# Optimization experiments

Measured on AMD Instinct MI355X. Metric: run time of the kernel, lower is better.

Reference implementation:

```python
import jax, jax.numpy as jnp
import numpy as np

B, N, H = 1048576, 6, 32

def setup_inputs() -> dict:
    key = jax.random.key(0)
    k = jax.random.split(key, 6)
    return {
        "x": jax.random.normal(k[0], (B, N), dtype=jnp.float32),
        "A_param": jax.random.normal(k[1], (N, N), dtype=jnp.float32),
        "W1": jax.random.normal(k[2], (H, 1), dtype=jnp.float32) * (1.0),  # Linear(1,H) weight
        "b1": jax.random.normal(k[3], (H,), dtype=jnp.float32) * 0.1,
        "W2": jax.random.normal(k[4], (1, H), dtype=jnp.float32) * (1.0 / np.sqrt(H)),
        "b2": jax.random.normal(k[5], (1,), dtype=jnp.float32) * 0.1,
    }

def reference(x, A_param, W1, b1, W2, b2):
    # A = softmax over rows of learned adjacency  [N, N]
    A = jax.nn.softmax(A_param, axis=-1)
    # fc1: per-node scalar -> hidden  [B, N, H]
    h = x[..., None] * W1[:, 0] + b1
    # graph mixing: A @ h  [B, N, H]
    h = jnp.einsum('mn,bnh->bmh', A, h)
    h = jax.nn.relu(h)
    # fc2: hidden -> scalar, squeeze  [B, N]
    h = jnp.einsum('bnh,h->bn', h, W2[0]) + b2[0]
    return x + h
```

## Files before the change

kernel.cpp:

```cpp
#include <hip/hip_runtime.h>
#include <math.h>


typedef float f32x2 __attribute__((ext_vector_type(2)));
typedef float f32x4 __attribute__((ext_vector_type(4)));

#define NN 6
#define HH 32
#define NB 512
#define YMIN  (-8.0f)
#define YSPAN (16.0f)
#define INVH  ((float)NB / YSPAN)
#define OFFS  (-YMIN * INVH)
#define BINW  (YSPAN / (float)NB)
#define WF4   192

#define LDS_FENCE() asm volatile("s_waitcnt lgkmcnt(0)" ::: "memory")

__device__ __forceinline__ f32x2 mk2(float a, float b) {
    f32x2 r; r.x = a; r.y = b; return r;
}

__device__ __forceinline__ f32x2 pk_fma(f32x2 a, f32x2 b, f32x2 c) {
#if __has_builtin(__builtin_elementwise_fma)
    return __builtin_elementwise_fma(a, b, c);
#else
    f32x2 r; r.x = fmaf(a.x, b.x, c.x); r.y = fmaf(a.y, b.y, c.y); return r;
#endif
}

__device__ __forceinline__ void eval_pair(
    f32x4 v0, f32x4 v1, f32x4 v2,
    const float* __restrict__ sA,
    const f32x2* __restrict__ sTab,
    f32x4& o0, f32x4& o1, f32x4& o2)
{
    f32x2 xx[NN];
    xx[0] = mk2(v0.x, v1.z);
    xx[1] = mk2(v0.y, v1.w);
    xx[2] = mk2(v0.z, v2.x);
    xx[3] = mk2(v0.w, v2.y);
    xx[4] = mk2(v1.x, v2.z);
    xx[5] = mk2(v1.y, v2.w);

    f32x2 yy[NN];
#pragma unroll
    for (int m = 0; m < NN; ++m) {
        f32x2 a = mk2(0.f, 0.f);
#pragma unroll
        for (int n = 0; n < NN; ++n) {
            float c = sA[m * NN + n];
            a = pk_fma(mk2(c, c), xx[n], a);
        }
        yy[m] = a;
    }

    f32x2 rr[NN];
#pragma unroll
    for (int m = 0; m < NN; ++m) {
#pragma unroll
        for (int half = 0; half < 2; ++half) {
            float yv = half ? yy[m].y : yy[m].x;
            float fi = fmaf(yv, INVH, OFFS);
            fi = fminf(fmaxf(fi, 0.0f), (float)(NB - 1));
            int k = (int)fi;
            f32x2 ab = sTab[k];
            float r = fmaf(ab.y, yv, ab.x);
            if (half) rr[m].y = r; else rr[m].x = r;
        }
    }

    o0.x = v0.x + rr[0].x;
    o0.y = v0.y + rr[1].x;
    o0.z = v0.z + rr[2].x;
    o0.w = v0.w + rr[3].x;
    o1.x = v1.x + rr[4].x;
    o1.y = v1.y + rr[5].x;
    o1.z = v1.z + rr[0].y;
    o1.w = v1.w + rr[1].y;
    o2.x = v2.x + rr[2].y;
    o2.y = v2.y + rr[3].y;
    o2.z = v2.z + rr[4].y;
    o2.w = v2.w + rr[5].y;
}

__global__ __launch_bounds__(256, 4) void graph_block_fused(
    const float* __restrict__ x,
    const float* __restrict__ Ap,
    const float* __restrict__ W1p,
    const float* __restrict__ b1p,
    const float* __restrict__ W2p,
    const float* __restrict__ b2p,
    float* __restrict__ out,
    int nF4)
{
    __shared__ float sA[NN * NN];
    __shared__ __align__(16) f32x2 sTab[NB];
    __shared__ __align__(16) f32x4 slab[4][WF4];

    const int tid = threadIdx.x;
    const int wid = tid >> 6;
    const int lane = tid & 63;

    const f32x4* __restrict__ xv = (const f32x4*)x;
    f32x4* __restrict__ ov = (f32x4*)out;

    const int base = (blockIdx.x * 4 + wid) * (2 * WF4);

    f32x4 a0, a1, a2, c0, c1, c2;
    if (base + lane < nF4)       a0 = xv[base + lane];
    if (base + 64 + lane < nF4)  a1 = xv[base + 64 + lane];
    if (base + 128 + lane < nF4) a2 = xv[base + 128 + lane];
    if (base + 192 + lane < nF4) c0 = xv[base + 192 + lane];
    if (base + 256 + lane < nF4) c1 = xv[base + 256 + lane];
    if (base + 320 + lane < nF4) c2 = xv[base + 320 + lane];

    if (tid < NN) {
        float r[NN];
        float mx = -INFINITY;
#pragma unroll
        for (int n = 0; n < NN; ++n) {
            r[n] = Ap[tid * NN + n];
            mx = fmaxf(mx, r[n]);
        }
        float s = 0.f;
#pragma unroll
        for (int n = 0; n < NN; ++n) {
            r[n] = expf(r[n] - mx);
            s += r[n];
        }
        float inv = 1.f / s;
#pragma unroll
        for (int n = 0; n < NN; ++n) sA[tid * NN + n] = r[n] * inv;
    }

    {
        float bb2 = b2p[0];
#pragma unroll
        for (int i = 0; i < 2; ++i) {
            int k = tid + i * 256;
            float ea = YMIN + (float)k * BINW;
            float eb = ea + BINW;
            float fa = bb2, fb = bb2;
#pragma unroll
            for (int h = 0; h < HH; ++h) {
                float w1 = W1p[h], bv = b1p[h], w2 = W2p[h];
                fa = fmaf(fmaxf(fmaf(w1, ea, bv), 0.f), w2, fa);
                fb = fmaf(fmaxf(fmaf(w1, eb, bv), 0.f), w2, fb);
            }
            float beta = (fb - fa) * INVH;
            sTab[k] = mk2(fmaf(-beta, ea, fa), beta);
        }
    }
    __syncthreads();

    f32x4* sl = slab[wid];

    auto run_chunk = [&](f32x4 s0, f32x4 s1, f32x4 s2, int cb) {
        sl[lane]       = s0;
        sl[64 + lane]  = s1;
        sl[128 + lane] = s2;
        LDS_FENCE();
        f32x4 v0 = sl[3 * lane];
        f32x4 v1 = sl[3 * lane + 1];
        f32x4 v2 = sl[3 * lane + 2];
        f32x4 o0, o1, o2;
        eval_pair(v0, v1, v2, sA, sTab, o0, o1, o2);
        LDS_FENCE();
        sl[3 * lane]     = o0;
        sl[3 * lane + 1] = o1;
        sl[3 * lane + 2] = o2;
        LDS_FENCE();
        f32x4 u0 = sl[lane];
        f32x4 u1 = sl[64 + lane];
        f32x4 u2 = sl[128 + lane];
        if (cb + lane < nF4)       ov[cb + lane] = u0;
        if (cb + 64 + lane < nF4)  ov[cb + 64 + lane] = u1;
        if (cb + 128 + lane < nF4) ov[cb + 128 + lane] = u2;
        LDS_FENCE();
    };

    run_chunk(a0, a1, a2, base);
    run_chunk(c0, c1, c2, base + WF4);
}

extern "C" void kernel_launch(void* const* d_in, const int* in_sizes, int n_in,
                              void* d_out, int out_size, void* d_ws, size_t ws_size,
                              hipStream_t stream) {
    const float* x  = (const float*)d_in[0];
    const float* Ap = (const float*)d_in[1];
    const float* W1 = (const float*)d_in[2];
    const float* b1 = (const float*)d_in[3];
    const float* W2 = (const float*)d_in[4];
    const float* b2 = (const float*)d_in[5];
    float* out = (float*)d_out;

    int nF4 = in_sizes[0] / 4;
    int perBlock = 4 * 2 * WF4;
    int grid = (nF4 + perBlock - 1) / perBlock;
    graph_block_fused<<<grid, 256, 0, stream>>>(x, Ap, W1, b1, W2, b2, out, nF4);
}
```

Measured before the change: 17.65 us.

## Split table/softmax prep into separate kernel and drop LDS transposition

Moves the softmax of the adjacency and the piecewise-linear lookup table construction into a one-block prep kernel that writes them to workspace. The main kernel then has each thread load its three float4 values directly (strided per-thread loads) and reads A and the table from global memory or cache instead of LDS. This removes the per-block table rebuild, the barrier and the LDS staging shuffle. In exchange it adds a second kernel launch, gather lookups that go through cache instead of LDS, and less coalesced 48-byte-strided loads.

```diff
diff --git a/kernel.cpp b/kernel.cpp
--- a/kernel.cpp
+++ b/kernel.cpp
@@ -13,9 +13,6 @@
 #define INVH  ((float)NB / YSPAN)
 #define OFFS  (-YMIN * INVH)
 #define BINW  (YSPAN / (float)NB)
-#define WF4   192
-
-#define LDS_FENCE() asm volatile("s_waitcnt lgkmcnt(0)" ::: "memory")
 
 __device__ __forceinline__ f32x2 mk2(float a, float b) {
     f32x2 r; r.x = a; r.y = b; return r;
@@ -29,91 +26,13 @@
 #endif
 }
 
-__device__ __forceinline__ void eval_pair(
-    f32x4 v0, f32x4 v1, f32x4 v2,
-    const float* __restrict__ sA,
-    const f32x2* __restrict__ sTab,
-    f32x4& o0, f32x4& o1, f32x4& o2)
-{
-    f32x2 xx[NN];
-    xx[0] = mk2(v0.x, v1.z);
-    xx[1] = mk2(v0.y, v1.w);
-    xx[2] = mk2(v0.z, v2.x);
-    xx[3] = mk2(v0.w, v2.y);
-    xx[4] = mk2(v1.x, v2.z);
-    xx[5] = mk2(v1.y, v2.w);
-
-    f32x2 yy[NN];
-#pragma unroll
-    for (int m = 0; m < NN; ++m) {
-        f32x2 a = mk2(0.f, 0.f);
-#pragma unroll
-        for (int n = 0; n < NN; ++n) {
-            float c = sA[m * NN + n];
-            a = pk_fma(mk2(c, c), xx[n], a);
-        }
-        yy[m] = a;
-    }
-
-    f32x2 rr[NN];
-#pragma unroll
-    for (int m = 0; m < NN; ++m) {
-#pragma unroll
-        for (int half = 0; half < 2; ++half) {
-            float yv = half ? yy[m].y : yy[m].x;
-            float fi = fmaf(yv, INVH, OFFS);
-            fi = fminf(fmaxf(fi, 0.0f), (float)(NB - 1));
-            int k = (int)fi;
-            f32x2 ab = sTab[k];
-            float r = fmaf(ab.y, yv, ab.x);
-            if (half) rr[m].y = r; else rr[m].x = r;
-        }
-    }
-
-    o0.x = v0.x + rr[0].x;
-    o0.y = v0.y + rr[1].x;
-    o0.z = v0.z + rr[2].x;
-    o0.w = v0.w + rr[3].x;
-    o1.x = v1.x + rr[4].x;
-    o1.y = v1.y + rr[5].x;
-    o1.z = v1.z + rr[0].y;
-    o1.w = v1.w + rr[1].y;
-    o2.x = v2.x + rr[2].y;
-    o2.y = v2.y + rr[3].y;
-    o2.z = v2.z + rr[4].y;
-    o2.w = v2.w + rr[5].y;
-}
-
-__global__ __launch_bounds__(256, 4) void graph_block_fused(
-    const float* __restrict__ x,
-    const float* __restrict__ Ap,
-    const float* __restrict__ W1p,
-    const float* __restrict__ b1p,
-    const float* __restrict__ W2p,
-    const float* __restrict__ b2p,
-    float* __restrict__ out,
-    int nF4)
-{
-    __shared__ float sA[NN * NN];
-    __shared__ __align__(16) f32x2 sTab[NB];
-    __shared__ __align__(16) f32x4 slab[4][WF4];
-
+__global__ void prep_kernel(const float* __restrict__ Ap,
+                            const float* __restrict__ W1p,
+                            const float* __restrict__ b1p,
+                            const float* __restrict__ W2p,
+                            const float* __restrict__ b2p,
+                            float* __restrict__ ws) {
     const int tid = threadIdx.x;
-    const int wid = tid >> 6;
-    const int lane = tid & 63;
-
-    const f32x4* __restrict__ xv = (const f32x4*)x;
-    f32x4* __restrict__ ov = (f32x4*)out;
-
-    const int base = (blockIdx.x * 4 + wid) * (2 * WF4);
-
-    f32x4 a0, a1, a2, c0, c1, c2;
-    if (base + lane < nF4)       a0 = xv[base + lane];
-    if (base + 64 + lane < nF4)  a1 = xv[base + 64 + lane];
-    if (base + 128 + lane < nF4) a2 = xv[base + 128 + lane];
-    if (base + 192 + lane < nF4) c0 = xv[base + 192 + lane];
-    if (base + 256 + lane < nF4) c1 = xv[base + 256 + lane];
-    if (base + 320 + lane < nF4) c2 = xv[base + 320 + lane];
 
     if (tid < NN) {
         float r[NN];
@@ -131,57 +50,99 @@
         }
         float inv = 1.f / s;
 #pragma unroll
-        for (int n = 0; n < NN; ++n) sA[tid * NN + n] = r[n] * inv;
+        for (int n = 0; n < NN; ++n) ws[tid * NN + n] = r[n] * inv;
     }
 
-    {
-        float bb2 = b2p[0];
+    float bb2 = b2p[0];
+    f32x2* __restrict__ tab = (f32x2*)(ws + 64);
 #pragma unroll
-        for (int i = 0; i < 2; ++i) {
-            int k = tid + i * 256;
-            float ea = YMIN + (float)k * BINW;
-            float eb = ea + BINW;
-            float fa = bb2, fb = bb2;
+    for (int i = 0; i < 2; ++i) {
+        int k = tid + i * 256;
+        float ea = YMIN + (float)k * BINW;
+        float eb = ea + BINW;
+        float fa = bb2, fb = bb2;
 #pragma unroll
-            for (int h = 0; h < HH; ++h) {
-                float w1 = W1p[h], bv = b1p[h], w2 = W2p[h];
-                fa = fmaf(fmaxf(fmaf(w1, ea, bv), 0.f), w2, fa);
-                fb = fmaf(fmaxf(fmaf(w1, eb, bv), 0.f), w2, fb);
-            }
-            float beta = (fb - fa) * INVH;
-            sTab[k] = mk2(fmaf(-beta, ea, fa), beta);
+        for (int h = 0; h < HH; ++h) {
+            float w1 = W1p[h], bv = b1p[h], w2 = W2p[h];
+            fa = fmaf(fmaxf(fmaf(w1, ea, bv), 0.f), w2, fa);
+            fb = fmaf(fmaxf(fmaf(w1, eb, bv), 0.f), w2, fb);
+        }
+        float beta = (fb - fa) * INVH;
+        tab[k] = mk2(fmaf(-beta, ea, fa), beta);
+    }
+}
+
+__global__ __launch_bounds__(256, 4) void graph_block_main(
+    const float* __restrict__ x,
+    const float* __restrict__ ws,
+    float* __restrict__ out,
+    int nPairs)
+{
+    const int p = blockIdx.x * 256 + threadIdx.x;
+    if (p >= nPairs) return;
+
+    const f32x4* __restrict__ xv = (const f32x4*)x;
+    f32x4* __restrict__ ov = (f32x4*)out;
+
+    f32x4 v0 = xv[3 * p];
+    f32x4 v1 = xv[3 * p + 1];
+    f32x4 v2 = xv[3 * p + 2];
+
+    const float* __restrict__ A = ws;
+    const f32x2* __restrict__ tab = (const f32x2*)(ws + 64);
+
+    f32x2 xx[NN];
+    xx[0] = mk2(v0.x, v1.z);
+    xx[1] = mk2(v0.y, v1.w);
+    xx[2] = mk2(v0.z, v2.x);
+    xx[3] = mk2(v0.w, v2.y);
+    xx[4] = mk2(v1.x, v2.z);
+    xx[5] = mk2(v1.y, v2.w);
+
+    f32x2 yy[NN];
+#pragma unroll
+    for (int m = 0; m < NN; ++m) {
+        f32x2 a = mk2(0.f, 0.f);
+#pragma unroll
+        for (int n = 0; n < NN; ++n) {
+            float c = A[m * NN + n];
+            a = pk_fma(mk2(c, c), xx[n], a);
+        }
+        yy[m] = a;
+    }
+
+    f32x2 rr[NN];
+#pragma unroll
+    for (int m = 0; m < NN; ++m) {
+#pragma unroll
+        for (int half = 0; half < 2; ++half) {
+            float yv = half ? yy[m].y : yy[m].x;
+            float fi = fmaf(yv, INVH, OFFS);
+            fi = fminf(fmaxf(fi, 0.0f), (float)(NB - 1));
+            int k = (int)fi;
+            f32x2 ab = tab[k];
+            float r = fmaf(ab.y, yv, ab.x);
+            if (half) rr[m].y = r; else rr[m].x = r;
         }
     }
-    __syncthreads();
 
-    f32x4* sl = slab[wid];
+    f32x4 o0, o1, o2;
+    o0.x = v0.x + rr[0].x;
+    o0.y = v0.y + rr[1].x;
+    o0.z = v0.z + rr[2].x;
+    o0.w = v0.w + rr[3].x;
+    o1.x = v1.x + rr[4].x;
+    o1.y = v1.y + rr[5].x;
+    o1.z = v1.z + rr[0].y;
+    o1.w = v1.w + rr[1].y;
+    o2.x = v2.x + rr[2].y;
+    o2.y = v2.y + rr[3].y;
+    o2.z = v2.z + rr[4].y;
+    o2.w = v2.w + rr[5].y;
 
-    auto run_chunk = [&](f32x4 s0, f32x4 s1, f32x4 s2, int cb) {
-        sl[lane]       = s0;
-        sl[64 + lane]  = s1;
-        sl[128 + lane] = s2;
-        LDS_FENCE();
-        f32x4 v0 = sl[3 * lane];
-        f32x4 v1 = sl[3 * lane + 1];
-        f32x4 v2 = sl[3 * lane + 2];
-        f32x4 o0, o1, o2;
-        eval_pair(v0, v1, v2, sA, sTab, o0, o1, o2);
-        LDS_FENCE();
-        sl[3 * lane]     = o0;
-        sl[3 * lane + 1] = o1;
-        sl[3 * lane + 2] = o2;
-        LDS_FENCE();
-        f32x4 u0 = sl[lane];
-        f32x4 u1 = sl[64 + lane];
-        f32x4 u2 = sl[128 + lane];
-        if (cb + lane < nF4)       ov[cb + lane] = u0;
-        if (cb + 64 + lane < nF4)  ov[cb + 64 + lane] = u1;
-        if (cb + 128 + lane < nF4) ov[cb + 128 + lane] = u2;
-        LDS_FENCE();
-    };
-
-    run_chunk(a0, a1, a2, base);
-    run_chunk(c0, c1, c2, base + WF4);
+    ov[3 * p]     = o0;
+    ov[3 * p + 1] = o1;
+    ov[3 * p + 2] = o2;
 }
 
 extern "C" void kernel_launch(void* const* d_in, const int* in_sizes, int n_in,
@@ -194,9 +155,11 @@
     const float* W2 = (const float*)d_in[4];
     const float* b2 = (const float*)d_in[5];
     float* out = (float*)d_out;
+    float* ws  = (float*)d_ws;
 
-    int nF4 = in_sizes[0] / 4;
-    int perBlock = 4 * 2 * WF4;
-    int grid = (nF4 + perBlock - 1) / perBlock;
-    graph_block_fused<<<grid, 256, 0, stream>>>(x, Ap, W1, b1, W2, b2, out, nF4);
+    prep_kernel<<<1, 256, 0, stream>>>(Ap, W1, b1, W2, b2, ws);
+
+    int nPairs = in_sizes[0] / 12;
+    int grid = (nPairs + 255) / 256;
+    graph_block_main<<<grid, 256, 0, stream>>>(x, ws, out, nPairs);
 }
```

Result: slower. 22.38 us (+26.8%).
